# Performance work log

Hardware: AMD Instinct MI355X
Metric: run time of the kernel (lower is better)

The kernel has to match this reference:

```python
import jax, jax.numpy as jnp
import numpy as np

K = 20
EPS = 1e-5
SLOPE = 0.2


def setup_inputs() -> dict:
    key = jax.random.key(0)
    k1, k2 = jax.random.split(key, 2)
    B, C, N, O = 2, 64, 8192, 64
    x = jax.random.normal(k1, (B, C, N), dtype=jnp.float32)
    W = jax.random.normal(k2, (O, 2 * C), dtype=jnp.float32) * 0.05  # Conv2d 1x1, bias=False
    gamma = jnp.ones((O,), dtype=jnp.float32)
    beta = jnp.zeros((O,), dtype=jnp.float32)
    return {"x": x, "W": W, "gamma": gamma, "beta": beta}


def reference(x, W, gamma, beta):
    # x: (B, C, N)
    B, C, N = x.shape
    xt = jnp.swapaxes(x, 1, 2)  # (B, N, C)

    # --- get_GraphFeatures: KNN by negative squared euclidean distance ---
    inner = jnp.einsum('bnc,bmc->bnm', xt, xt)          # (B, N, N)
    sq = jnp.sum(xt * xt, axis=-1)                      # (B, N)
    neg_dist = 2.0 * inner - sq[:, :, None] - sq[:, None, :]
    _, idx = jax.lax.top_k(neg_dist, K)                 # (B, N, K) int32

    # gather neighbor features: (B, N, K, C)
    nbr = jax.vmap(lambda pts, i: pts[i])(xt, idx)
    center = xt[:, :, None, :]                          # (B, N, 1, C)
    # edge feature: concat(x_j - x_i, x_i) -> (B, N, K, 2C)
    edge = jnp.concatenate([nbr - center, jnp.broadcast_to(center, nbr.shape)], axis=-1)

    # --- 1x1 conv (pointwise GEMM) -> (B, O, N, K) ---
    h = jnp.einsum('bnkf,of->bonk', edge, W)

    # --- BatchNorm2d (training-mode batch stats over B, N, K per channel) ---
    mean = jnp.mean(h, axis=(0, 2, 3), keepdims=True)
    var = jnp.var(h, axis=(0, 2, 3), keepdims=True)
    h = (h - mean) * jax.lax.rsqrt(var + EPS)
    h = h * gamma[None, :, None, None] + beta[None, :, None, None]

    # --- LeakyReLU(0.2) + max over neighbors ---
    h = jnp.where(h >= 0, h, SLOPE * h)
    return jnp.max(h, axis=-1)                          # (B, O, N)
```

## Files before the change

### kernel.cpp

```cpp
#include <hip/hip_runtime.h>
#include <cfloat>

#define BB 2
#define NN 8192
#define OO 64
#define KK 20
#define QB 128
#define MS 16
#define CHUNK 512
#define CAPQ 192
#define RB 8
#define RBS 9

using f16x8  = __attribute__((ext_vector_type(8))) _Float16;
using f32x16 = __attribute__((ext_vector_type(16))) float;
typedef unsigned long long u64;

#define XH_OFF ((size_t)0)
#define XL_OFF (XH_OFF + (size_t)BB*NN*32)
#define SQ_OFF (XL_OFF + (size_t)BB*NN*32)
#define Y1_OFF (SQ_OFF + (size_t)BB*NN)
#define Y2_OFF (Y1_OFF + (size_t)BB*NN*64)
#define TH_OFF (Y2_OFF + (size_t)BB*NN*64)
#define CN_OFF (TH_OFF + (size_t)BB*NN)
#define TL_OFF (CN_OFF + (size_t)BB*NN)
#define CA_OFF (TL_OFF + (size_t)2*BB*NN*KK)
#define IX_OFF (CA_OFF + (size_t)BB*NN*CAPQ*2)
#define HX_OFF (IX_OFF + (size_t)BB*NN*KK)
#define HN_OFF (HX_OFF + (size_t)BB*NN*64)
#define ST_OFF (HN_OFF + (size_t)BB*NN*64)

__device__ __forceinline__ size_t frag_off(int b, int tile, int t, int lane) {
    return ((((size_t)b * (NN / 32) + tile) * 4 + t) * 64 + lane) * 8;
}

__device__ __forceinline__ unsigned fmap(float f) {
    unsigned u = __float_as_uint(f);
    return (u & 0x80000000u) ? ~u : (u | 0x80000000u);
}

__device__ __forceinline__ void sort16(float* v) {
#pragma unroll
    for (int k = 2; k <= 16; k <<= 1) {
#pragma unroll
        for (int j = k >> 1; j > 0; j >>= 1) {
#pragma unroll
            for (int i = 0; i < 16; ++i) {
                int l = i ^ j;
                if (l > i) {
                    bool up = ((i & k) == 0);
                    float mn = fminf(v[i], v[l]);
                    float mx = fmaxf(v[i], v[l]);
                    v[i] = up ? mn : mx;
                    v[l] = up ? mx : mn;
                }
            }
        }
    }
}
__device__ __forceinline__ void bmerge32(float* A) {
#pragma unroll
    for (int j = 16; j > 0; j >>= 1) {
#pragma unroll
        for (int i = 0; i < 32; ++i) {
            if ((i & j) == 0) {
                float mn = fminf(A[i], A[i | j]);
                float mx = fmaxf(A[i], A[i | j]);
                A[i] = mn;
                A[i | j] = mx;
            }
        }
    }
}
__device__ __forceinline__ void merge32_16(float* A, const float* B) {
#pragma unroll
    for (int i = 16; i < 32; ++i) A[i] = fminf(A[i], B[31 - i]);
    bmerge32(A);
}
__device__ __forceinline__ void merge32_32(float* A, const float* B) {
    float t[32];
#pragma unroll
    for (int i = 0; i < 32; ++i) t[i] = fminf(A[i], B[31 - i]);
    bmerge32(t);
#pragma unroll
    for (int i = 0; i < 32; ++i) A[i] = t[i];
}

__device__ __forceinline__ void load_atile(const _Float16* __restrict__ xh,
                                           const _Float16* __restrict__ xl,
                                           int b, int ptile, int lane,
                                           f16x8* Ah, f16x8* Al) {
#pragma unroll
    for (int t = 0; t < 4; ++t) {
        size_t o = frag_off(b, ptile, t, lane);
        Ah[t] = *(const f16x8*)&xh[o];
        Al[t] = *(const f16x8*)&xl[o];
    }
}

__device__ __forceinline__ void dist_from_frags(const f16x8* Ah, const f16x8* Al,
                                                const float* sqs, int sbase, int kh,
                                                const f16x8* Qh, const f16x8* Ql,
                                                float* dv) {
    f32x16 c0, c1;
#pragma unroll
    for (int r2 = 0; r2 < 4; ++r2) {
        float4 sv = *(const float4*)&sqs[sbase + 8 * r2 + 4 * kh];
        c0[4 * r2 + 0] = sv.x;
        c0[4 * r2 + 1] = sv.y;
        c0[4 * r2 + 2] = sv.z;
        c0[4 * r2 + 3] = sv.w;
    }
#pragma unroll
    for (int i = 0; i < 16; ++i) c1[i] = 0.f;
#pragma unroll
    for (int t = 0; t < 4; ++t) {
        c0 = __builtin_amdgcn_mfma_f32_32x32x16_f16(Ah[t], Qh[t], c0, 0, 0, 0);
        c1 = __builtin_amdgcn_mfma_f32_32x32x16_f16(Ah[t], Ql[t], c1, 0, 0, 0);
        c1 = __builtin_amdgcn_mfma_f32_32x32x16_f16(Al[t], Qh[t], c1, 0, 0, 0);
    }
#pragma unroll
    for (int i = 0; i < 16; ++i)
        dv[i] = fmaf(-2.f, c0[i], -9.765625e-4f * c1[i]);
}

__device__ __forceinline__ void load_qfrag(const _Float16* __restrict__ xh,
                                           const _Float16* __restrict__ xl,
                                           int b, int qbase, int lane,
                                           f16x8* Qh, f16x8* Ql) {
    const int qtile = qbase >> 5;
#pragma unroll
    for (int t = 0; t < 4; ++t) {
        size_t o = frag_off(b, qtile, t, lane);
        Qh[t] = *(const f16x8*)&xh[o];
        Ql[t] = *(const f16x8*)&xl[o];
    }
}

__global__ void __launch_bounds__(256, 2)
kA(const float* __restrict__ x, const float* __restrict__ W,
   float* __restrict__ ws) {
    __shared__ __align__(16) float w1s[32 * 64];
    __shared__ __align__(16) float w2s[32 * 64];
    __shared__ float xs[64 * 65];
    __shared__ float tb[64 * 33];
    const int bb = blockIdx.z;
    const int og = blockIdx.y;
    const int obase = og * 32;
    const int nbase = blockIdx.x * 64;
    const int tn = threadIdx.x & 63, tq = threadIdx.x >> 6;

    for (int i = threadIdx.x; i < 2048; i += 256) {
        int ol = i >> 6, c = i & 63;
        float a = W[(obase + ol) * 128 + c];
        float d = W[(obase + ol) * 128 + 64 + c];
        w1s[i] = a;
        w2s[i] = d - a;
    }
    for (int i = threadIdx.x; i < 4096; i += 256) {
        int c = i >> 6, nl = i & 63;
        xs[c * 65 + nl] = x[((size_t)bb * 64 + c) * NN + nbase + nl];
    }
    if (og == 0) {
        if (blockIdx.x == 0 && bb == 0 && threadIdx.x < 128)
            ws[ST_OFF + threadIdx.x] = 0.f;
        int gid = (bb * 128 + blockIdx.x) * 256 + threadIdx.x;
        if (gid < BB * NN) ((int*)(ws + CN_OFF))[gid] = 0;
    }
    __syncthreads();

    float xc[64];
#pragma unroll
    for (int c = 0; c < 64; ++c) xc[c] = xs[c * 65 + tn];

    if (og == 0 && tq == 0) {
        float sqv = 0.f;
#pragma unroll
        for (int c = 0; c < 64; ++c) sqv = fmaf(xc[c], xc[c], sqv);
        int n = nbase + tn;
        ws[SQ_OFF + (size_t)bb * NN + n] = sqv;
        _Float16* xh = (_Float16*)(ws + XH_OFF);
        _Float16* xl = (_Float16*)(ws + XL_OFF);
        int tile = n >> 5, r = n & 31;
#pragma unroll
        for (int t = 0; t < 4; ++t) {
#pragma unroll
            for (int kh = 0; kh < 2; ++kh) {
                f16x8 vh, vl;
#pragma unroll
                for (int j = 0; j < 8; ++j) {
                    float v = xc[t * 16 + kh * 8 + j];
                    _Float16 h = (_Float16)v;
                    vh[j] = h;
                    vl[j] = (_Float16)((v - (float)h) * 2048.f);
                }
                size_t o = frag_off(bb, tile, t, kh * 32 + r);
                *(f16x8*)&xh[o] = vh;
                *(f16x8*)&xl[o] = vl;
            }
        }
    }

    float a1v[8], a2v[8];
#pragma unroll
    for (int o2 = 0; o2 < 8; ++o2) {
        int ol = tq * 8 + o2;
        const float4* w1v = (const float4*)&w1s[ol * 64];
        const float4* w2v = (const float4*)&w2s[ol * 64];
        float a1 = 0.f, a2 = 0.f;
#pragma unroll
        for (int c4 = 0; c4 < 16; ++c4) {
            float4 v1 = w1v[c4];
            float4 v2 = w2v[c4];
            a1 = fmaf(v1.x, xc[4*c4],   a1);
            a1 = fmaf(v1.y, xc[4*c4+1], a1);
            a1 = fmaf(v1.z, xc[4*c4+2], a1);
            a1 = fmaf(v1.w, xc[4*c4+3], a1);
            a2 = fmaf(v2.x, xc[4*c4],   a2);
            a2 = fmaf(v2.y, xc[4*c4+1], a2);
            a2 = fmaf(v2.z, xc[4*c4+2], a2);
            a2 = fmaf(v2.w, xc[4*c4+3], a2);
        }
        a1v[o2] = a1;
        a2v[o2] = a2;
    }

    const int lo = threadIdx.x & 31;
    const int lp = (threadIdx.x >> 5) & 1;
#pragma unroll
    for (int o2 = 0; o2 < 8; ++o2)
        tb[tn * 33 + tq * 8 + o2] = a1v[o2];
    __syncthreads();
#pragma unroll
    for (int j = 0; j < 8; ++j) {
        int r = tq * 16 + 2 * j + lp;
        ws[Y1_OFF + ((size_t)bb * NN + nbase + r) * 64 + obase + lo] = tb[r * 33 + lo];
    }
    __syncthreads();
#pragma unroll
    for (int o2 = 0; o2 < 8; ++o2)
        tb[tn * 33 + tq * 8 + o2] = a2v[o2];
    __syncthreads();
#pragma unroll
    for (int j = 0; j < 8; ++j) {
        int r = tq * 16 + 2 * j + lp;
        ws[Y2_OFF + ((size_t)bb * NN + nbase + r) * 64 + obase + lo] = tb[r * 33 + lo];
    }
}

__global__ void __launch_bounds__(256, 3)
kT(const _Float16* __restrict__ xh, const _Float16* __restrict__ xl,
   const float* __restrict__ sq, float* __restrict__ thrL) {
    __shared__ float mrg[32 * 128];
    __shared__ __align__(16) float sqs[1024];
    const int tid  = threadIdx.x;
    const int lane = tid & 63;
    const int wv   = tid >> 6;
    const int qcol = lane & 31;
    const int kh   = lane >> 5;
    const int b     = blockIdx.y >> 1;
    const int s     = blockIdx.y & 1;
    const int qbase = blockIdx.x * 32;

    for (int i = tid; i < 1024; i += 256)
        sqs[i] = -0.5f * sq[(size_t)b * NN + s * 1024 + i];

    f16x8 Qh[4], Ql[4];
    load_qfrag(xh, xl, b, qbase, lane, Qh, Ql);
    __syncthreads();

    float dk[32];
#pragma unroll
    for (int i = 0; i < 32; ++i) dk[i] = FLT_MAX;

    const int p0 = s * 1024 + wv * 256;
    for (int pt = p0; pt < p0 + 256; pt += 32) {
        f16x8 Ah[4], Al[4];
        load_atile(xh, xl, b, pt >> 5, lane, Ah, Al);
        float dv[16];
        dist_from_frags(Ah, Al, sqs, pt - s * 1024, kh, Qh, Ql, dv);
        float m16 = dv[0];
#pragma unroll
        for (int i = 1; i < 16; ++i) m16 = fminf(m16, dv[i]);
        if (__any(m16 < dk[KK - 1])) {
            sort16(dv);
            merge32_16(dk, dv);
        }
    }

    {
        float B[32];
#pragma unroll
        for (int j = 0; j < 32; ++j) B[j] = __shfl(dk[j], lane | 32);
        merge32_32(dk, B);
    }
    if (kh == 0) {
#pragma unroll
        for (int j = 0; j < 32; ++j) mrg[j * 128 + wv * 32 + qcol] = dk[j];
    }
    __syncthreads();

    if (tid < 32) {
        float B[32];
#pragma unroll 1
        for (int w = 1; w < 4; ++w) {
#pragma unroll
            for (int j = 0; j < 32; ++j) B[j] = mrg[j * 128 + w * 32 + tid];
            merge32_32(dk, B);
        }
        size_t base = (((size_t)b * 2 + s) * NN + qbase + tid) * KK;
#pragma unroll
        for (int j = 0; j < KK; ++j) thrL[base + j] = dk[j];
    }
}

__global__ void kM2(const float* __restrict__ thrL, float* __restrict__ thr) {
    int gid = blockIdx.x * 256 + threadIdx.x;
    int b = gid >> 13, q = gid & (NN - 1);
    float A[KK], Bv[KK];
    const float4* pa = (const float4*)&thrL[(((size_t)b * 2 + 0) * NN + q) * KK];
    const float4* pb = (const float4*)&thrL[(((size_t)b * 2 + 1) * NN + q) * KK];
#pragma unroll
    for (int i = 0; i < 5; ++i) {
        float4 va = pa[i];
        float4 vb = pb[i];
        A[4*i] = va.x;  A[4*i+1] = va.y;  A[4*i+2] = va.z;  A[4*i+3] = va.w;
        Bv[4*i] = vb.x; Bv[4*i+1] = vb.y; Bv[4*i+2] = vb.z; Bv[4*i+3] = vb.w;
    }
    float v = fminf(Bv[KK - 1], A[KK - 1]);
#pragma unroll
    for (int i = 1; i < KK; ++i)
        v = fminf(v, fmaxf(A[i - 1], Bv[KK - 1 - i]));
    thr[gid] = v + fabsf(v) * 1e-6f + 1e-6f;
}

__global__ void __launch_bounds__(256, 4)
kS(const _Float16* __restrict__ xh, const _Float16* __restrict__ xl,
   const float* __restrict__ sq, const float* __restrict__ thr,
   int* __restrict__ cnt, u64* __restrict__ cand) {
    __shared__ u64 lbuf[256 * RBS];
    __shared__ __align__(16) float sqs[CHUNK];
    const int tid  = threadIdx.x;
    const int lane = tid & 63;
    const int wv   = tid >> 6;
    const int qcol = lane & 31;
    const int kh   = lane >> 5;
    const int id     = blockIdx.x;
    const int ychunk = id & 15;
    const int qt     = (id >> 4) & 63;
    const int b      = (id >> 10) & 1;
    const int qbase  = qt * QB + wv * 32;
    const int pbase0 = ychunk * CHUNK;
    const int ptile0 = pbase0 >> 5;

    for (int i = tid; i < CHUNK; i += 256)
        sqs[i] = -0.5f * sq[(size_t)b * NN + pbase0 + i];

    f16x8 Qh[4], Ql[4];
    load_qfrag(xh, xl, b, qbase, lane, Qh, Ql);

    const size_t qidx = (size_t)b * NN + qbase + qcol;
    const float tv = thr[qidx];
    const size_t cb = qidx * CAPQ;
    int c_ = 0;

    __syncthreads();

    auto flushS = [&]() {
        if (c_ > 0) {
            int base = atomicAdd(&cnt[qidx], c_);
#pragma unroll 1
            for (int j = 0; j < c_; ++j) {
                int slot = base + j;
                if (slot < CAPQ) cand[cb + slot] = lbuf[tid * RBS + j];
            }
            c_ = 0;
        }
    };

#pragma unroll 2
    for (int tt = 0; tt < CHUNK / 32; ++tt) {
        f16x8 Ah[4], Al[4];
        load_atile(xh, xl, b, ptile0 + tt, lane, Ah, Al);
        float dv[16];
        dist_from_frags(Ah, Al, sqs, tt * 32, kh, Qh, Ql, dv);

        const int pb4 = pbase0 + tt * 32 + 4 * kh;
#pragma unroll
        for (int i = 0; i < 16; ++i) {
            float d = dv[i];
            if (d <= tv) {
                int id2 = pb4 + ((i & 3) + 8 * (i >> 2));
                lbuf[tid * RBS + c_] = ((u64)fmap(d) << 32) | (unsigned)id2;
                if (++c_ == RB) flushS();
            }
        }
    }
    flushS();
}

__global__ void __launch_bounds__(256, 4)
kP(const int* __restrict__ cnt, const u64* __restrict__ cand,
   int* __restrict__ idxK) {
    const int lane = threadIdx.x & 63;
    const int wq   = threadIdx.x >> 6;
    const int q    = blockIdx.x * 4 + wq;
    int m = cnt[q];
    m = m < CAPQ ? m : CAPQ;
    const u64* cp = &cand[(size_t)q * CAPQ];

    u64 v0 = (lane       < m) ? cp[lane]       : ~0ull;
    u64 v1 = (lane + 64  < m) ? cp[lane + 64]  : ~0ull;
    u64 v2 = (lane + 128 < m) ? cp[lane + 128] : ~0ull;
    int r0 = 0, r1 = 0, r2 = 0;

    {
        const int cap0 = m < 64 ? m : 64;
#pragma unroll 4
        for (int jj = 0; jj < cap0; ++jj) {
            u64 bv = __shfl(v0, jj);
            r0 += (bv < v0); r1 += (bv < v1); r2 += (bv < v2);
        }
    }
    if (m > 64) {
        const int cap1 = (m - 64) < 64 ? (m - 64) : 64;
#pragma unroll 4
        for (int jj = 0; jj < cap1; ++jj) {
            u64 bv = __shfl(v1, jj);
            r0 += (bv < v0); r1 += (bv < v1); r2 += (bv < v2);
        }
    }
    if (m > 128) {
        const int cap2 = (m - 128) < 64 ? (m - 128) : 64;
#pragma unroll 4
        for (int jj = 0; jj < cap2; ++jj) {
            u64 bv = __shfl(v2, jj);
            r0 += (bv < v0); r1 += (bv < v1); r2 += (bv < v2);
        }
    }

    int* op = &idxK[(size_t)q * KK];
    if (lane       < m && r0 < KK) op[r0] = (int)(unsigned)(v0 & 0xffffffffu);
    if (lane + 64  < m && r1 < KK) op[r1] = (int)(unsigned)(v1 & 0xffffffffu);
    if (lane + 128 < m && r2 < KK) op[r2] = (int)(unsigned)(v2 & 0xffffffffu);
}

__global__ void kC1(const float* __restrict__ y1, const float* __restrict__ y2,
                    const int* __restrict__ idxK, float* __restrict__ hmaxT,
                    float* __restrict__ hminT, float* __restrict__ stats) {
    __shared__ int li[32 * KK];
    __shared__ float red[256];
    __shared__ float thm[32 * 65];
    __shared__ float thn[32 * 65];
    int b = blockIdx.y;
    int o = threadIdx.x & 63;
    int nn = threadIdx.x >> 6;
    int nbase = blockIdx.x * 32;

    for (int i = threadIdx.x; i < 32 * KK; i += 256)
        li[i] = idxK[((size_t)b * NN + nbase) * KK + i];
    __syncthreads();

    float s = 0.f, ss = 0.f;
    for (int gidx = 0; gidx < 8; ++gidx) {
        int nl = gidx * 4 + nn;
        int n = nbase + nl;
        float y2v = y2[((size_t)b * NN + n) * 64 + o];
        float hm = -FLT_MAX, hn = FLT_MAX;
        const int* lin = &li[nl * KK];
#pragma unroll 4
        for (int k = 0; k < KK; ++k) {
            int j = lin[k];
            float h = y1[((size_t)b * NN + j) * 64 + o] + y2v;
            s += h;
            ss += h * h;
            hm = fmaxf(hm, h);
            hn = fminf(hn, h);
        }
        thm[nl * 65 + o] = hm;
        thn[nl * 65 + o] = hn;
    }
    __syncthreads();

    int l = threadIdx.x & 31, g = threadIdx.x >> 5;
#pragma unroll
    for (int i = 0; i < 8; ++i) {
        int o2 = g * 8 + i;
        hmaxT[((size_t)b * 64 + o2) * NN + nbase + l] = thm[l * 65 + o2];
        hminT[((size_t)b * 64 + o2) * NN + nbase + l] = thn[l * 65 + o2];
    }

    __syncthreads();
    red[threadIdx.x] = s;
    __syncthreads();
    if (threadIdx.x < 64) {
        float v = red[o] + red[64 + o] + red[128 + o] + red[192 + o];
        atomicAdd(&stats[o], v);
    }
    __syncthreads();
    red[threadIdx.x] = ss;
    __syncthreads();
    if (threadIdx.x < 64) {
        float v = red[o] + red[64 + o] + red[128 + o] + red[192 + o];
        atomicAdd(&stats[64 + o], v);
    }
}

__global__ void kC3(const float* __restrict__ hmaxT, const float* __restrict__ hminT,
                    const float* __restrict__ stats, const float* __restrict__ gamma,
                    const float* __restrict__ beta, float* __restrict__ out) {
    int o = blockIdx.x;
    int half = blockIdx.y;
    int b = blockIdx.z;
    const float c = (float)BB * NN * KK;
    float mean = stats[o] / c;
    float var = stats[64 + o] / c - mean * mean;
    float rs = rsqrtf(var + 1e-5f);
    float a = gamma[o] * rs;
    float b2 = beta[o] - a * mean;
    size_t rowb = ((size_t)b * 64 + o) * NN;
    int n0 = half * (NN / 2), n1 = n0 + NN / 2;
    for (int n = n0 + threadIdx.x; n < n1; n += 256) {
        float hm = hmaxT[rowb + n];
        float hn = hminT[rowb + n];
        float hs = (a >= 0.f) ? hm : hn;
        float v = a * hs + b2;
        v = (v >= 0.f) ? v : 0.2f * v;
        out[rowb + n] = v;
    }
}

extern "C" void kernel_launch(void* const* d_in, const int* in_sizes, int n_in,
                              void* d_out, int out_size, void* d_ws, size_t ws_size,
                              hipStream_t stream) {
    const float* x     = (const float*)d_in[0];
    const float* W     = (const float*)d_in[1];
    const float* gamma = (const float*)d_in[2];
    const float* beta  = (const float*)d_in[3];
    float* out = (float*)d_out;
    float* ws  = (float*)d_ws;

    _Float16* xh = (_Float16*)(ws + XH_OFF);
    _Float16* xl = (_Float16*)(ws + XL_OFF);
    float* sq    = ws + SQ_OFF;
    float* y1    = ws + Y1_OFF;
    float* y2    = ws + Y2_OFF;
    float* thr   = ws + TH_OFF;
    int*   cnt   = (int*)(ws + CN_OFF);
    float* thrL  = ws + TL_OFF;
    u64*   cand  = (u64*)(ws + CA_OFF);
    int*   idxK  = (int*)(ws + IX_OFF);
    float* hmaxT = ws + HX_OFF;
    float* hminT = ws + HN_OFF;
    float* stats = ws + ST_OFF;

    kA<<<dim3(NN / 64, 2, BB), 256, 0, stream>>>(x, W, ws);
    kT<<<dim3(NN / 32, 2 * BB), 256, 0, stream>>>(xh, xl, sq, thrL);
    kM2<<<dim3(BB * NN / 256), 256, 0, stream>>>(thrL, thr);
    kS<<<dim3(MS * (NN / QB) * BB), 256, 0, stream>>>(xh, xl, sq, thr, cnt, cand);
    kP<<<dim3(BB * NN / 4), 256, 0, stream>>>(cnt, cand, idxK);
    kC1<<<dim3(NN / 32, BB), 256, 0, stream>>>(y1, y2, idxK, hmaxT, hminT, stats);
    kC3<<<dim3(OO, 2, BB), 256, 0, stream>>>(hmaxT, hminT, stats, gamma, beta, out);
}
```

Measured before the change: 250.7 us.

## Fold threshold merge into kT and candidate ranking into kC1

kT now covers the 2048-point sample per batch in a single block instead of two halves, so it writes the final per-query threshold directly and the kM2 merge kernel and its thrL buffer go away. The kP ranking kernel is folded into kC1: each wavefront ranks the candidates for 8 queries and writes the top-K indices straight into shared memory, so the idxK global round trip is gone. This removes two launches and some global traffic. In exchange kT launches half as many blocks, each doing twice the serial work, and kC1 now runs the shuffle-based ranking before its gather, which may lengthen that kernel.

```diff
diff --git a/kernel.cpp b/kernel.cpp
--- a/kernel.cpp
+++ b/kernel.cpp
@@ -250,20 +250,19 @@
 
 __global__ void __launch_bounds__(256, 3)
 kT(const _Float16* __restrict__ xh, const _Float16* __restrict__ xl,
-   const float* __restrict__ sq, float* __restrict__ thrL) {
+   const float* __restrict__ sq, float* __restrict__ thr) {
     __shared__ float mrg[32 * 128];
-    __shared__ __align__(16) float sqs[1024];
+    __shared__ __align__(16) float sqs[2048];
     const int tid  = threadIdx.x;
     const int lane = tid & 63;
     const int wv   = tid >> 6;
     const int qcol = lane & 31;
     const int kh   = lane >> 5;
-    const int b     = blockIdx.y >> 1;
-    const int s     = blockIdx.y & 1;
+    const int b     = blockIdx.y;
     const int qbase = blockIdx.x * 32;
 
-    for (int i = tid; i < 1024; i += 256)
-        sqs[i] = -0.5f * sq[(size_t)b * NN + s * 1024 + i];
+    for (int i = tid; i < 2048; i += 256)
+        sqs[i] = -0.5f * sq[(size_t)b * NN + i];
 
     f16x8 Qh[4], Ql[4];
     load_qfrag(xh, xl, b, qbase, lane, Qh, Ql);
@@ -273,12 +272,12 @@
 #pragma unroll
     for (int i = 0; i < 32; ++i) dk[i] = FLT_MAX;
 
-    const int p0 = s * 1024 + wv * 256;
-    for (int pt = p0; pt < p0 + 256; pt += 32) {
+    const int p0 = wv * 512;
+    for (int pt = p0; pt < p0 + 512; pt += 32) {
         f16x8 Ah[4], Al[4];
         load_atile(xh, xl, b, pt >> 5, lane, Ah, Al);
         float dv[16];
-        dist_from_frags(Ah, Al, sqs, pt - s * 1024, kh, Qh, Ql, dv);
+        dist_from_frags(Ah, Al, sqs, pt, kh, Qh, Ql, dv);
         float m16 = dv[0];
 #pragma unroll
         for (int i = 1; i < 16; ++i) m16 = fminf(m16, dv[i]);
@@ -308,30 +307,9 @@
             for (int j = 0; j < 32; ++j) B[j] = mrg[j * 128 + w * 32 + tid];
             merge32_32(dk, B);
         }
-        size_t base = (((size_t)b * 2 + s) * NN + qbase + tid) * KK;
-#pragma unroll
-        for (int j = 0; j < KK; ++j) thrL[base + j] = dk[j];
-    }
-}
-
-__global__ void kM2(const float* __restrict__ thrL, float* __restrict__ thr) {
-    int gid = blockIdx.x * 256 + threadIdx.x;
-    int b = gid >> 13, q = gid & (NN - 1);
-    float A[KK], Bv[KK];
-    const float4* pa = (const float4*)&thrL[(((size_t)b * 2 + 0) * NN + q) * KK];
-    const float4* pb = (const float4*)&thrL[(((size_t)b * 2 + 1) * NN + q) * KK];
-#pragma unroll
-    for (int i = 0; i < 5; ++i) {
-        float4 va = pa[i];
-        float4 vb = pb[i];
-        A[4*i] = va.x;  A[4*i+1] = va.y;  A[4*i+2] = va.z;  A[4*i+3] = va.w;
-        Bv[4*i] = vb.x; Bv[4*i+1] = vb.y; Bv[4*i+2] = vb.z; Bv[4*i+3] = vb.w;
-    }
-    float v = fminf(Bv[KK - 1], A[KK - 1]);
-#pragma unroll
-    for (int i = 1; i < KK; ++i)
-        v = fminf(v, fmaxf(A[i - 1], Bv[KK - 1 - i]));
-    thr[gid] = v + fabsf(v) * 1e-6f + 1e-6f;
+        float v = dk[KK - 1];
+        thr[(size_t)b * NN + qbase + tid] = v + fabsf(v) * 1e-6f + 1e-6f;
+    }
 }
 
 __global__ void __launch_bounds__(256, 4)
@@ -399,55 +377,10 @@
     flushS();
 }
 
-__global__ void __launch_bounds__(256, 4)
-kP(const int* __restrict__ cnt, const u64* __restrict__ cand,
-   int* __restrict__ idxK) {
-    const int lane = threadIdx.x & 63;
-    const int wq   = threadIdx.x >> 6;
-    const int q    = blockIdx.x * 4 + wq;
-    int m = cnt[q];
-    m = m < CAPQ ? m : CAPQ;
-    const u64* cp = &cand[(size_t)q * CAPQ];
-
-    u64 v0 = (lane       < m) ? cp[lane]       : ~0ull;
-    u64 v1 = (lane + 64  < m) ? cp[lane + 64]  : ~0ull;
-    u64 v2 = (lane + 128 < m) ? cp[lane + 128] : ~0ull;
-    int r0 = 0, r1 = 0, r2 = 0;
-
-    {
-        const int cap0 = m < 64 ? m : 64;
-#pragma unroll 4
-        for (int jj = 0; jj < cap0; ++jj) {
-            u64 bv = __shfl(v0, jj);
-            r0 += (bv < v0); r1 += (bv < v1); r2 += (bv < v2);
-        }
-    }
-    if (m > 64) {
-        const int cap1 = (m - 64) < 64 ? (m - 64) : 64;
-#pragma unroll 4
-        for (int jj = 0; jj < cap1; ++jj) {
-            u64 bv = __shfl(v1, jj);
-            r0 += (bv < v0); r1 += (bv < v1); r2 += (bv < v2);
-        }
-    }
-    if (m > 128) {
-        const int cap2 = (m - 128) < 64 ? (m - 128) : 64;
-#pragma unroll 4
-        for (int jj = 0; jj < cap2; ++jj) {
-            u64 bv = __shfl(v2, jj);
-            r0 += (bv < v0); r1 += (bv < v1); r2 += (bv < v2);
-        }
-    }
-
-    int* op = &idxK[(size_t)q * KK];
-    if (lane       < m && r0 < KK) op[r0] = (int)(unsigned)(v0 & 0xffffffffu);
-    if (lane + 64  < m && r1 < KK) op[r1] = (int)(unsigned)(v1 & 0xffffffffu);
-    if (lane + 128 < m && r2 < KK) op[r2] = (int)(unsigned)(v2 & 0xffffffffu);
-}
-
 __global__ void kC1(const float* __restrict__ y1, const float* __restrict__ y2,
-                    const int* __restrict__ idxK, float* __restrict__ hmaxT,
-                    float* __restrict__ hminT, float* __restrict__ stats) {
+                    const int* __restrict__ cnt, const u64* __restrict__ cand,
+                    float* __restrict__ hmaxT, float* __restrict__ hminT,
+                    float* __restrict__ stats) {
     __shared__ int li[32 * KK];
     __shared__ float red[256];
     __shared__ float thm[32 * 65];
@@ -456,9 +389,47 @@
     int o = threadIdx.x & 63;
     int nn = threadIdx.x >> 6;
     int nbase = blockIdx.x * 32;
-
-    for (int i = threadIdx.x; i < 32 * KK; i += 256)
-        li[i] = idxK[((size_t)b * NN + nbase) * KK + i];
+    const int lane = threadIdx.x & 63;
+
+#pragma unroll 1
+    for (int qq = 0; qq < 8; ++qq) {
+        const int nl = nn * 8 + qq;
+        const size_t q = (size_t)b * NN + nbase + nl;
+        int m = cnt[q];
+        m = m < CAPQ ? m : CAPQ;
+        const u64* cp = &cand[q * CAPQ];
+        u64 v0 = (lane       < m) ? cp[lane]       : ~0ull;
+        u64 v1 = (lane + 64  < m) ? cp[lane + 64]  : ~0ull;
+        u64 v2 = (lane + 128 < m) ? cp[lane + 128] : ~0ull;
+        int r0 = 0, r1 = 0, r2 = 0;
+        {
+            const int cap0 = m < 64 ? m : 64;
+#pragma unroll 4
+            for (int jj = 0; jj < cap0; ++jj) {
+                u64 bv = __shfl(v0, jj);
+                r0 += (bv < v0); r1 += (bv < v1); r2 += (bv < v2);
+            }
+        }
+        if (m > 64) {
+            const int cap1 = (m - 64) < 64 ? (m - 64) : 64;
+#pragma unroll 4
+            for (int jj = 0; jj < cap1; ++jj) {
+                u64 bv = __shfl(v1, jj);
+                r0 += (bv < v0); r1 += (bv < v1); r2 += (bv < v2);
+            }
+        }
+        if (m > 128) {
+            const int cap2 = (m - 128) < 64 ? (m - 128) : 64;
+#pragma unroll 4
+            for (int jj = 0; jj < cap2; ++jj) {
+                u64 bv = __shfl(v2, jj);
+                r0 += (bv < v0); r1 += (bv < v1); r2 += (bv < v2);
+            }
+        }
+        if (lane       < m && r0 < KK) li[nl * KK + r0] = (int)(unsigned)(v0 & 0xffffffffu);
+        if (lane + 64  < m && r1 < KK) li[nl * KK + r1] = (int)(unsigned)(v1 & 0xffffffffu);
+        if (lane + 128 < m && r2 < KK) li[nl * KK + r2] = (int)(unsigned)(v2 & 0xffffffffu);
+    }
     __syncthreads();
 
     float s = 0.f, ss = 0.f;
@@ -547,18 +518,14 @@
     float* y2    = ws + Y2_OFF;
     float* thr   = ws + TH_OFF;
     int*   cnt   = (int*)(ws + CN_OFF);
-    float* thrL  = ws + TL_OFF;
     u64*   cand  = (u64*)(ws + CA_OFF);
-    int*   idxK  = (int*)(ws + IX_OFF);
     float* hmaxT = ws + HX_OFF;
     float* hminT = ws + HN_OFF;
     float* stats = ws + ST_OFF;
 
     kA<<<dim3(NN / 64, 2, BB), 256, 0, stream>>>(x, W, ws);
-    kT<<<dim3(NN / 32, 2 * BB), 256, 0, stream>>>(xh, xl, sq, thrL);
-    kM2<<<dim3(BB * NN / 256), 256, 0, stream>>>(thrL, thr);
+    kT<<<dim3(NN / 32, BB), 256, 0, stream>>>(xh, xl, sq, thr);
     kS<<<dim3(MS * (NN / QB) * BB), 256, 0, stream>>>(xh, xl, sq, thr, cnt, cand);
-    kP<<<dim3(BB * NN / 4), 256, 0, stream>>>(cnt, cand, idxK);
-    kC1<<<dim3(NN / 32, BB), 256, 0, stream>>>(y1, y2, idxK, hmaxT, hminT, stats);
+    kC1<<<dim3(NN / 32, BB), 256, 0, stream>>>(y1, y2, cnt, cand, hmaxT, hminT, stats);
     kC3<<<dim3(OO, 2, BB), 256, 0, stream>>>(hmaxT, hminT, stats, gamma, beta, out);
 }
```

Result: slower. 269.5 us (+7.5%).
